# Kernel tuning notes

Measured on AMD Instinct MI355X. Metric: run time of the kernel, lower is better.

## Reference

```python
import math
import jax, jax.numpy as jnp
import numpy as np

B, N, M = 8, 2048, 1024
INPUT_SIZE = 512
HEAD_DIM = 64
NUM_HEADS = 6
ATTN_SIZE = HEAD_DIM * NUM_HEADS
MAX_CLASSES = 512


def setup_inputs() -> dict:
    key = jax.random.key(0)
    k1, k2, k3, k4, k5, k6, k7 = jax.random.split(key, 7)
    bound = 1.0 / math.sqrt(INPUT_SIZE)
    return {
        "train_embeddings": jax.random.normal(k1, (B, N, INPUT_SIZE), jnp.float32),
        "test_embeddings": jax.random.normal(k2, (B, M, INPUT_SIZE), jnp.float32),
        "targets": jax.random.randint(k3, (B, N), 0, MAX_CLASSES),
        # torch nn.Linear weights, stored as [in, out] for direct matmul
        "Wq": jax.random.uniform(k4, (INPUT_SIZE, ATTN_SIZE), jnp.float32, -bound, bound),
        "bq": jax.random.uniform(k5, (ATTN_SIZE,), jnp.float32, -bound, bound),
        "Wk": jax.random.uniform(k6, (INPUT_SIZE, ATTN_SIZE), jnp.float32, -bound, bound),
        "bk": jax.random.uniform(k7, (ATTN_SIZE,), jnp.float32, -bound, bound),
    }


def reference(train_embeddings, test_embeddings, targets, Wq, bq, Wk, bk):
    b, m, _ = test_embeddings.shape
    # projections -> [B, S, H, D]
    q_bmhd = (test_embeddings @ Wq + bq).reshape(b, m, NUM_HEADS, HEAD_DIM)
    k_bnhd = (train_embeddings @ Wk + bk).reshape(b, -1, NUM_HEADS, HEAD_DIM)
    scale = 1.0 / math.sqrt(HEAD_DIM)  # SDPA default scale
    # attention scores [B, H, M, N]
    scores = jnp.einsum("bmhd,bnhd->bhmn", q_bmhd, k_bnhd) * scale
    attn = jax.nn.softmax(scores, axis=-1)
    # one-hot train targets [B, N, C]; chunk-folding in the torch code is a
    # memory trick — mathematically it is just attn @ one_hot per head
    onehot_bnc = jax.nn.one_hot(targets, MAX_CLASSES, dtype=q_bmhd.dtype)
    out_bhmc = jnp.einsum("bhmn,bnc->bhmc", attn, onehot_bnc)
    out_bmc = out_bhmc.mean(axis=1)          # mean over heads
    out_mbc = out_bmc.transpose(1, 0, 2)      # [M, B, C]
    return jnp.log(jnp.clip(out_mbc, 1e-05) + 3e-05)
```

## Files before the change

### kernel.cpp

```cpp
#include <hip/hip_runtime.h>
#include <hip/hip_bf16.h>

#define BQ 8
#define NN 2048
#define MM 1024
#define EE 512
#define NH 6
#define AA 384
#define CC 512

#define KROW_B (AA * 2)
#define TILE_B (16 * KROW_B)
#define STILE_B (32 * KROW_B)
#define WROW_B (EE * 2)
#define WTILE_B (16 * WROW_B)

#define QSCALE 0.1803368801111204f

typedef __bf16 bf16x8 __attribute__((ext_vector_type(8)));
typedef float  f32x4  __attribute__((ext_vector_type(4)));
using bf16 = __hip_bfloat16;

static __device__ __forceinline__ f32x4 mfma16(bf16x8 a, bf16x8 b, f32x4 c) {
  return __builtin_amdgcn_mfma_f32_16x16x32_bf16(a, b, c, 0, 0, 0);
}

typedef __attribute__((address_space(1))) const void gconst_void;
typedef __attribute__((address_space(3))) void lds_void_t;
static __device__ __forceinline__ void ld_lds16(const void* g, void* l) {
  __builtin_amdgcn_global_load_lds((gconst_void*)g, (lds_void_t*)l, 16, 0, 0);
}

static __device__ __forceinline__ unsigned short f2bfu(float x) {
  union { __hip_bfloat16 h; unsigned short u; } v;
  v.h = __float2bfloat16(x);
  return v.u;
}
static __device__ __forceinline__ float bf2f(unsigned short u) {
  union { unsigned int i; float f; } x;
  x.i = ((unsigned int)u) << 16;
  return x.f;
}

__global__ __launch_bounds__(256) void transw_kernel(const float* __restrict__ W, bf16* __restrict__ WT) {
  __shared__ float t[64][65];
  int kb = (blockIdx.x / 6) * 64, nb = (blockIdx.x % 6) * 64;
  int tid = threadIdx.x;
  int lr = tid >> 4, lc = (tid & 15) * 4;
  #pragma unroll
  for (int p = 0; p < 4; p++) {
    int k = lr + p * 16;
    float4 v = *reinterpret_cast<const float4*>(W + (size_t)(kb + k) * AA + nb + lc);
    t[k][lc] = v.x; t[k][lc + 1] = v.y; t[k][lc + 2] = v.z; t[k][lc + 3] = v.w;
  }
  __syncthreads();
  #pragma unroll
  for (int p = 0; p < 4; p++) {
    int n = lr + p * 16;
    bf16* dst = WT + (size_t)(nb + n) * EE + kb + lc;
    dst[0] = __float2bfloat16(t[lc][n]);
    dst[1] = __float2bfloat16(t[lc + 1][n]);
    dst[2] = __float2bfloat16(t[lc + 2][n]);
    dst[3] = __float2bfloat16(t[lc + 3][n]);
  }
}

__global__ __launch_bounds__(512) void build_kernel(const int* __restrict__ targets,
                                                    int* __restrict__ offs, int* __restrict__ idxs) {
  __shared__ int cnt[CC], ssum[CC], pos[CC];
  int b = blockIdx.x, tid = threadIdx.x;
  cnt[tid] = 0;
  __syncthreads();
  int t[4];
  #pragma unroll
  for (int i = 0; i < 4; i++) {
    t[i] = targets[b * NN + tid * 4 + i];
    atomicAdd(&cnt[t[i]], 1);
  }
  __syncthreads();
  ssum[tid] = cnt[tid];
  __syncthreads();
  for (int d = 1; d < CC; d <<= 1) {
    int v = (tid >= d) ? ssum[tid - d] : 0;
    __syncthreads();
    ssum[tid] += v;
    __syncthreads();
  }
  int excl = ssum[tid] - cnt[tid];
  offs[b * (CC + 1) + tid] = excl;
  if (tid == CC - 1) offs[b * (CC + 1) + CC] = NN;
  pos[tid] = excl;
  __syncthreads();
  #pragma unroll
  for (int i = 0; i < 4; i++) {
    int p = atomicAdd(&pos[t[i]], 1);
    idxs[b * NN + p] = tid * 4 + i;
  }
}

__global__ __launch_bounds__(256, 3) void proj_kernel(
    const float* __restrict__ test, const float* __restrict__ train,
    const bf16* __restrict__ WqT, const bf16* __restrict__ WkT,
    const float* __restrict__ bq, const float* __restrict__ bk,
    bf16* __restrict__ Qb, bf16* __restrict__ Kb)
{
  __shared__ char wbuf[3][WTILE_B];
  int tid = threadIdx.x, wid = tid >> 6, lane = tid & 63;
  int bid = blockIdx.x;
  int sub = bid & 1, unit = bid >> 1;
  const float* A; const bf16* WT; const float* bias; bf16* C; float scale; int m0;
  if (unit < 128) { A = test;  WT = WqT; bias = bq; C = Qb; scale = QSCALE; m0 = unit * 64; }
  else            { A = train; WT = WkT; bias = bk; C = Kb; scale = 1.0f;   m0 = (unit - 128) * 64; }
  m0 += wid * 16;
  int row = lane & 15, hi = lane >> 4;

  bf16x8 af[16];
  const float* arow = A + (size_t)(m0 + row) * EE + hi * 8;
  #pragma unroll
  for (int ks = 0; ks < 16; ks++) {
    float4 u = *reinterpret_cast<const float4*>(arow + ks * 32);
    float4 v = *reinterpret_cast<const float4*>(arow + ks * 32 + 4);
    bf16x8 f;
    f[0] = (__bf16)u.x; f[1] = (__bf16)u.y; f[2] = (__bf16)u.z; f[3] = (__bf16)u.w;
    f[4] = (__bf16)v.x; f[5] = (__bf16)v.y; f[6] = (__bf16)v.z; f[7] = (__bf16)v.w;
    af[ks] = f;
  }

  int ldso[4], srco[4];
  #pragma unroll
  for (int i = 0; i < 4; i++) {
    int off = tid * 16 + i * 4096;
    int rw = off >> 10, c = off & 1023;
    ldso[i] = off;
    srco[i] = rw * WROW_B + (c ^ ((rw & 7) << 4));
  }
  const char* wgbase = (const char*)WT + (size_t)sub * 12 * WTILE_B;
  int sw = (row & 7) << 4;

  auto stage = [&](int t, int buf) {
    const char* src = wgbase + (size_t)t * WTILE_B;
    #pragma unroll
    for (int i = 0; i < 4; i++) ld_lds16(src + srco[i], wbuf[buf] + ldso[i]);
  };
  auto compute = [&](int buf, int t) {
    const char* wb = wbuf[buf] + row * WROW_B;
    f32x4 acc0 = {0.f, 0.f, 0.f, 0.f}, acc1 = {0.f, 0.f, 0.f, 0.f};
    #pragma unroll
    for (int ks = 0; ks < 16; ks += 2) {
      bf16x8 w0 = *reinterpret_cast<const bf16x8*>(wb + ((hi * 16 + ks * 64) ^ sw));
      bf16x8 w1 = *reinterpret_cast<const bf16x8*>(wb + ((hi * 16 + (ks + 1) * 64) ^ sw));
      acc0 = mfma16(af[ks], w0, acc0);
      acc1 = mfma16(af[ks + 1], w1, acc1);
    }
    f32x4 acc = acc0 + acc1;
    int ocol = (sub * 12 + t) * 16 + row;
    float bv = bias[ocol];
    #pragma unroll
    for (int j = 0; j < 4; j++)
      C[(size_t)(m0 + hi * 4 + j) * AA + ocol] = __float2bfloat16((acc[j] + bv) * scale);
  };

  stage(0, 0);
  stage(1, 1);
  asm volatile("s_waitcnt vmcnt(4)" ::: "memory");
  __builtin_amdgcn_s_barrier();
  __builtin_amdgcn_sched_barrier(0);
  stage(2, 2);
  compute(0, 0);

  int cur = 1, stg = 0;
  #pragma unroll 1
  for (int t = 1; t < 11; t++) {
    asm volatile("s_waitcnt vmcnt(8)" ::: "memory");
    __builtin_amdgcn_s_barrier();
    __builtin_amdgcn_sched_barrier(0);
    if (t < 10) stage(t + 2, stg);
    compute(cur, t);
    cur = cur + 1 < 3 ? cur + 1 : 0;
    stg = stg + 1 < 3 ? stg + 1 : 0;
  }
  asm volatile("s_waitcnt vmcnt(4)" ::: "memory");
  __builtin_amdgcn_s_barrier();
  __builtin_amdgcn_sched_barrier(0);
  compute(cur, 11);
}

__global__ __launch_bounds__(256, 3) void zpass_kernel(
    const bf16* __restrict__ Qb, const bf16* __restrict__ Kb, float* __restrict__ Zp)
{
  __shared__ char kbuf[2][STILE_B];
  int id = blockIdx.x;
  int b = id & 7, r = id >> 3, mt = r & 15, nc = r >> 4;
  int tid = threadIdx.x, wid = tid >> 6, lane = tid & 63;
  int m0 = mt * 64 + wid * 16, n0 = nc * 256;
  int row = lane & 15, hi = lane >> 4;

  bf16x8 qf[12];
  const bf16* qrow = Qb + ((size_t)(b * MM + m0 + row)) * AA + hi * 8;
  #pragma unroll
  for (int ks = 0; ks < 12; ks++) qf[ks] = *reinterpret_cast<const bf16x8*>(qrow + ks * 32);

  int ldso[6], srco[6];
  #pragma unroll
  for (int i = 0; i < 6; i++) {
    int off = tid * 16 + i * 4096;
    int rw = off / KROW_B, c = off - rw * KROW_B;
    ldso[i] = off;
    srco[i] = rw * KROW_B + (c ^ ((rw & 7) << 4));
  }
  const char* kgbase = (const char*)(Kb + ((size_t)(b * NN + n0)) * AA);

  int sw = (row & 7) << 4;
  int rbase = row * KROW_B;
  int x0 = rbase + ((hi * 16) ^ sw);
  int x1 = rbase + (((hi * 16) + 64) ^ sw);

  float zacc[NH][4];
  #pragma unroll
  for (int h = 0; h < NH; h++)
    #pragma unroll
    for (int j = 0; j < 4; j++) zacc[h][j] = 0.f;

  auto stage = [&](int t, int buf) {
    const char* src = kgbase + (size_t)t * STILE_B;
    #pragma unroll
    for (int i = 0; i < 6; i++) ld_lds16(src + srco[i], kbuf[buf] + ldso[i]);
  };
  auto compute = [&](int buf) {
    __builtin_amdgcn_s_setprio(1);
    #pragma unroll
    for (int s = 0; s < 2; s++) {
      const char* kb = kbuf[buf] + s * TILE_B;
      #pragma unroll
      for (int h = 0; h < NH; h++) {
        bf16x8 k0 = *reinterpret_cast<const bf16x8*>(kb + h * 128 + x0);
        bf16x8 k1 = *reinterpret_cast<const bf16x8*>(kb + h * 128 + x1);
        f32x4 acc = {0.f, 0.f, 0.f, 0.f};
        acc = mfma16(qf[2 * h], k0, acc);
        acc = mfma16(qf[2 * h + 1], k1, acc);
        #pragma unroll
        for (int j = 0; j < 4; j++) zacc[h][j] += __builtin_amdgcn_exp2f(acc[j]);
      }
    }
    __builtin_amdgcn_s_setprio(0);
  };

  stage(0, 0);
  asm volatile("s_waitcnt vmcnt(0)" ::: "memory");
  __builtin_amdgcn_s_barrier();
  __builtin_amdgcn_sched_barrier(0);
  stage(1, 1);
  compute(0);

  #pragma unroll 1
  for (int i = 1; i < 8; i++) {
    asm volatile("s_waitcnt vmcnt(0)" ::: "memory");
    __builtin_amdgcn_s_barrier();
    __builtin_amdgcn_sched_barrier(0);
    if (i < 7) stage(i + 1, (i + 1) & 1);
    compute(i & 1);
  }

  #pragma unroll
  for (int h = 0; h < NH; h++)
    #pragma unroll
    for (int j = 0; j < 4; j++) {
      float v = zacc[h][j];
      v += __shfl_xor(v, 1); v += __shfl_xor(v, 2);
      v += __shfl_xor(v, 4); v += __shfl_xor(v, 8);
      zacc[h][j] = v;
    }
  if (row == 0) {
    #pragma unroll
    for (int h = 0; h < NH; h++)
      #pragma unroll
      for (int j = 0; j < 4; j++)
        Zp[(((size_t)nc * 8 + b) * NH + h) * MM + m0 + hi * 4 + j] = zacc[h][j];
  }
}

__global__ __launch_bounds__(256, 3) void wpass_kernel(
    const bf16* __restrict__ Qb, const bf16* __restrict__ Kb,
    const float* __restrict__ Zp, bf16* __restrict__ W2)
{
  __shared__ char kbuf[2][STILE_B];
  int id = blockIdx.x;
  int b = id & 7, r = id >> 3, mt = r & 15, nc = r >> 4;
  int tid = threadIdx.x, wid = tid >> 6, lane = tid & 63;
  int m0 = mt * 64 + wid * 16, n0 = nc * 256;
  int row = lane & 15, hi = lane >> 4;

  bf16x8 qf[12];
  const bf16* qrow = Qb + ((size_t)(b * MM + m0 + row)) * AA + hi * 8;
  #pragma unroll
  for (int ks = 0; ks < 12; ks++) qf[ks] = *reinterpret_cast<const bf16x8*>(qrow + ks * 32);

  float rz[NH][4];
  #pragma unroll
  for (int h = 0; h < NH; h++) {
    f32x4 z = {0.f, 0.f, 0.f, 0.f};
    #pragma unroll
    for (int p = 0; p < 8; p++)
      z += *reinterpret_cast<const f32x4*>(Zp + (((size_t)p * 8 + b) * NH + h) * MM + m0 + hi * 4);
    #pragma unroll
    for (int j = 0; j < 4; j++) rz[h][j] = 1.0f / (6.0f * z[j]);
  }

  int ldso[6], srco[6];
  #pragma unroll
  for (int i = 0; i < 6; i++) {
    int off = tid * 16 + i * 4096;
    int rw = off / KROW_B, c = off - rw * KROW_B;
    ldso[i] = off;
    srco[i] = rw * KROW_B + (c ^ ((rw & 7) << 4));
  }
  const char* kgbase = (const char*)(Kb + ((size_t)(b * NN + n0)) * AA);

  int sw = (row & 7) << 4;
  int rbase = row * KROW_B;
  int x0 = rbase + ((hi * 16) ^ sw);
  int x1 = rbase + (((hi * 16) + 64) ^ sw);

  int m4 = (m0 >> 2) + hi;

  auto stage = [&](int t, int buf) {
    const char* src = kgbase + (size_t)t * STILE_B;
    #pragma unroll
    for (int i = 0; i < 6; i++) ld_lds16(src + srco[i], kbuf[buf] + ldso[i]);
  };
  auto compute = [&](int buf, int st) {
    #pragma unroll
    for (int s = 0; s < 2; s++) {
      const char* kb = kbuf[buf] + s * TILE_B;
      __builtin_amdgcn_s_setprio(1);
      float w0 = 0.f, w1 = 0.f, w2 = 0.f, w3 = 0.f;
      #pragma unroll
      for (int h = 0; h < NH; h++) {
        bf16x8 k0 = *reinterpret_cast<const bf16x8*>(kb + h * 128 + x0);
        bf16x8 k1 = *reinterpret_cast<const bf16x8*>(kb + h * 128 + x1);
        f32x4 acc = {0.f, 0.f, 0.f, 0.f};
        acc = mfma16(qf[2 * h], k0, acc);
        acc = mfma16(qf[2 * h + 1], k1, acc);
        w0 += __builtin_amdgcn_exp2f(acc[0]) * rz[h][0];
        w1 += __builtin_amdgcn_exp2f(acc[1]) * rz[h][1];
        w2 += __builtin_amdgcn_exp2f(acc[2]) * rz[h][2];
        w3 += __builtin_amdgcn_exp2f(acc[3]) * rz[h][3];
      }
      __builtin_amdgcn_s_setprio(0);
      int n = n0 + (st * 2 + s) * 16 + row;
      ushort4 q;
      q.x = f2bfu(w0); q.y = f2bfu(w1); q.z = f2bfu(w2); q.w = f2bfu(w3);
      *reinterpret_cast<ushort4*>((unsigned short*)W2 + (((size_t)(b * 256 + m4)) * NN + n) * 4) = q;
    }
  };

  stage(0, 0);
  asm volatile("s_waitcnt vmcnt(0)" ::: "memory");
  __builtin_amdgcn_s_barrier();
  __builtin_amdgcn_sched_barrier(0);
  stage(1, 1);
  compute(0, 0);

  #pragma unroll 1
  for (int i = 1; i < 8; i++) {
    asm volatile("s_waitcnt vmcnt(2)" ::: "memory");
    __builtin_amdgcn_s_barrier();
    __builtin_amdgcn_sched_barrier(0);
    if (i < 7) stage(i + 1, (i + 1) & 1);
    compute(i & 1, i);
  }
}

__global__ __launch_bounds__(512) void gather_kernel(
    const bf16* __restrict__ W2, const int* __restrict__ offs,
    const int* __restrict__ idxs, float* __restrict__ out)
{
  __shared__ char wl[2 * NN * 8];
  __shared__ int ilb[NN];
  int id = blockIdx.x;
  int b = id & 7, mt = id >> 3;
  int g0 = mt * 2;
  int tid = threadIdx.x;

  const uint4* src = (const uint4*)((const unsigned short*)W2 + ((size_t)(b * 256 + g0)) * NN * 4);
  uint4* dst = (uint4*)wl;
  #pragma unroll
  for (int i = tid; i < 2 * NN * 8 / 16; i += 512) dst[i] = src[i];
  const int* il = idxs + b * NN;
  #pragma unroll
  for (int i = tid; i < NN; i += 512) ilb[i] = il[i];
  __syncthreads();

  int c = tid;
  int o0 = offs[b * (CC + 1) + c], o1 = offs[b * (CC + 1) + c + 1];
  #pragma unroll 1
  for (int g = 0; g < 2; g++) {
    float s0 = 0.f, s1 = 0.f, s2 = 0.f, s3 = 0.f;
    for (int i = o0; i < o1; i++) {
      int idx = ilb[i];
      ushort4 v = *reinterpret_cast<const ushort4*>(wl + g * (NN * 8) + idx * 8);
      s0 += bf2f(v.x); s1 += bf2f(v.y); s2 += bf2f(v.z); s3 += bf2f(v.w);
    }
    int m = mt * 8 + g * 4;
    out[((size_t)(m + 0) * BQ + b) * CC + c] = __logf(fmaxf(s0, 1e-5f) + 3e-5f);
    out[((size_t)(m + 1) * BQ + b) * CC + c] = __logf(fmaxf(s1, 1e-5f) + 3e-5f);
    out[((size_t)(m + 2) * BQ + b) * CC + c] = __logf(fmaxf(s2, 1e-5f) + 3e-5f);
    out[((size_t)(m + 3) * BQ + b) * CC + c] = __logf(fmaxf(s3, 1e-5f) + 3e-5f);
  }
}

extern "C" void kernel_launch(void* const* d_in, const int* in_sizes, int n_in,
                              void* d_out, int out_size, void* d_ws, size_t ws_size,
                              hipStream_t stream) {
  const float* train = (const float*)d_in[0];
  const float* test  = (const float*)d_in[1];
  const int*   tgt   = (const int*)d_in[2];
  const float* Wq    = (const float*)d_in[3];
  const float* bq    = (const float*)d_in[4];
  const float* Wk    = (const float*)d_in[5];
  const float* bk    = (const float*)d_in[6];
  float* out = (float*)d_out;

  char* ws = (char*)d_ws;
  bf16*  WqT  = (bf16*)(ws);
  bf16*  WkT  = (bf16*)(ws + 393216);
  bf16*  Qb   = (bf16*)(ws + 786432);
  bf16*  Kb   = (bf16*)(ws + 7077888);
  float* Zp   = (float*)(ws + 19660800);
  bf16*  Wbuf = (bf16*)(ws + 21233664);
  int*   offs = (int*)(ws + 54788096);
  int*   idxs = (int*)(ws + 54804512);

  transw_kernel<<<48, 256, 0, stream>>>(Wq, WqT);
  transw_kernel<<<48, 256, 0, stream>>>(Wk, WkT);
  build_kernel<<<BQ, 512, 0, stream>>>(tgt, offs, idxs);
  proj_kernel<<<768, 256, 0, stream>>>(test, train, WqT, WkT, bq, bk, Qb, Kb);
  zpass_kernel<<<1024, 256, 0, stream>>>(Qb, Kb, Zp);
  wpass_kernel<<<1024, 256, 0, stream>>>(Qb, Kb, Zp, Wbuf);
  gather_kernel<<<1024, 512, 0, stream>>>(Wbuf, offs, idxs, out);
}
```

Measured before the change: 112.3 us.

## Double per-wave M rows in zpass/wpass to reuse K tiles; merge transpose launches

Each wave in zpass and wpass now covers 32 query rows instead of 16. It holds two sets of Q fragments and reuses every K fragment read from LDS for two MFMAs, so the grid halves and LDS and global K traffic per output falls. The two weight-transpose launches are merged into a single 96-block launch to save one launch. In exchange, register pressure rises (launch bounds drop to 2 blocks per CU), there are fewer blocks to fill the GPU, and the wpass wait count is relaxed to match the extra stores.

```diff
diff --git a/kernel.cpp b/kernel.cpp
--- a/kernel.cpp
+++ b/kernel.cpp
@@ -42,9 +42,15 @@
   return x.f;
 }
 
-__global__ __launch_bounds__(256) void transw_kernel(const float* __restrict__ W, bf16* __restrict__ WT) {
+__global__ __launch_bounds__(256) void transw_kernel(
+    const float* __restrict__ Wq, const float* __restrict__ Wk,
+    bf16* __restrict__ WqT, bf16* __restrict__ WkT) {
   __shared__ float t[64][65];
-  int kb = (blockIdx.x / 6) * 64, nb = (blockIdx.x % 6) * 64;
+  int id = blockIdx.x;
+  const float* W = (id < 48) ? Wq : Wk;
+  bf16* WT = (id < 48) ? WqT : WkT;
+  if (id >= 48) id -= 48;
+  int kb = (id / 6) * 64, nb = (id % 6) * 64;
   int tid = threadIdx.x;
   int lr = tid >> 4, lc = (tid & 15) * 4;
   #pragma unroll
@@ -185,20 +191,23 @@
   compute(cur, 11);
 }
 
-__global__ __launch_bounds__(256, 3) void zpass_kernel(
+__global__ __launch_bounds__(256, 2) void zpass_kernel(
     const bf16* __restrict__ Qb, const bf16* __restrict__ Kb, float* __restrict__ Zp)
 {
   __shared__ char kbuf[2][STILE_B];
   int id = blockIdx.x;
-  int b = id & 7, r = id >> 3, mt = r & 15, nc = r >> 4;
+  int b = id & 7, r = id >> 3, mt = r & 7, nc = r >> 3;
   int tid = threadIdx.x, wid = tid >> 6, lane = tid & 63;
-  int m0 = mt * 64 + wid * 16, n0 = nc * 256;
+  int m0 = mt * 128 + wid * 32, n0 = nc * 256;
   int row = lane & 15, hi = lane >> 4;
 
-  bf16x8 qf[12];
-  const bf16* qrow = Qb + ((size_t)(b * MM + m0 + row)) * AA + hi * 8;
-  #pragma unroll
-  for (int ks = 0; ks < 12; ks++) qf[ks] = *reinterpret_cast<const bf16x8*>(qrow + ks * 32);
+  bf16x8 qf[2][12];
+  #pragma unroll
+  for (int s = 0; s < 2; s++) {
+    const bf16* qrow = Qb + ((size_t)(b * MM + m0 + s * 16 + row)) * AA + hi * 8;
+    #pragma unroll
+    for (int ks = 0; ks < 12; ks++) qf[s][ks] = *reinterpret_cast<const bf16x8*>(qrow + ks * 32);
+  }
 
   int ldso[6], srco[6];
   #pragma unroll
@@ -215,11 +224,13 @@
   int x0 = rbase + ((hi * 16) ^ sw);
   int x1 = rbase + (((hi * 16) + 64) ^ sw);
 
-  float zacc[NH][4];
-  #pragma unroll
-  for (int h = 0; h < NH; h++)
-    #pragma unroll
-    for (int j = 0; j < 4; j++) zacc[h][j] = 0.f;
+  float zacc[2][NH][4];
+  #pragma unroll
+  for (int s = 0; s < 2; s++)
+    #pragma unroll
+    for (int h = 0; h < NH; h++)
+      #pragma unroll
+      for (int j = 0; j < 4; j++) zacc[s][h][j] = 0.f;
 
   auto stage = [&](int t, int buf) {
     const char* src = kgbase + (size_t)t * STILE_B;
@@ -229,17 +240,22 @@
   auto compute = [&](int buf) {
     __builtin_amdgcn_s_setprio(1);
     #pragma unroll
-    for (int s = 0; s < 2; s++) {
-      const char* kb = kbuf[buf] + s * TILE_B;
+    for (int sub = 0; sub < 2; sub++) {
+      const char* kb = kbuf[buf] + sub * TILE_B;
       #pragma unroll
       for (int h = 0; h < NH; h++) {
         bf16x8 k0 = *reinterpret_cast<const bf16x8*>(kb + h * 128 + x0);
         bf16x8 k1 = *reinterpret_cast<const bf16x8*>(kb + h * 128 + x1);
-        f32x4 acc = {0.f, 0.f, 0.f, 0.f};
-        acc = mfma16(qf[2 * h], k0, acc);
-        acc = mfma16(qf[2 * h + 1], k1, acc);
+        f32x4 a0 = {0.f, 0.f, 0.f, 0.f}, a1 = {0.f, 0.f, 0.f, 0.f};
+        a0 = mfma16(qf[0][2 * h], k0, a0);
+        a1 = mfma16(qf[1][2 * h], k0, a1);
+        a0 = mfma16(qf[0][2 * h + 1], k1, a0);
+        a1 = mfma16(qf[1][2 * h + 1], k1, a1);
         #pragma unroll
-        for (int j = 0; j < 4; j++) zacc[h][j] += __builtin_amdgcn_exp2f(acc[j]);
+        for (int j = 0; j < 4; j++) {
+          zacc[0][h][j] += __builtin_amdgcn_exp2f(a0[j]);
+          zacc[1][h][j] += __builtin_amdgcn_exp2f(a1[j]);
+        }
       }
     }
     __builtin_amdgcn_s_setprio(0);
@@ -262,49 +278,58 @@
   }
 
   #pragma unroll
-  for (int h = 0; h < NH; h++)
-    #pragma unroll
-    for (int j = 0; j < 4; j++) {
-      float v = zacc[h][j];
-      v += __shfl_xor(v, 1); v += __shfl_xor(v, 2);
-      v += __shfl_xor(v, 4); v += __shfl_xor(v, 8);
-      zacc[h][j] = v;
-    }
+  for (int s = 0; s < 2; s++)
+    #pragma unroll
+    for (int h = 0; h < NH; h++)
+      #pragma unroll
+      for (int j = 0; j < 4; j++) {
+        float v = zacc[s][h][j];
+        v += __shfl_xor(v, 1); v += __shfl_xor(v, 2);
+        v += __shfl_xor(v, 4); v += __shfl_xor(v, 8);
+        zacc[s][h][j] = v;
+      }
   if (row == 0) {
     #pragma unroll
-    for (int h = 0; h < NH; h++)
-      #pragma unroll
-      for (int j = 0; j < 4; j++)
-        Zp[(((size_t)nc * 8 + b) * NH + h) * MM + m0 + hi * 4 + j] = zacc[h][j];
-  }
-}
-
-__global__ __launch_bounds__(256, 3) void wpass_kernel(
+    for (int s = 0; s < 2; s++)
+      #pragma unroll
+      for (int h = 0; h < NH; h++)
+        #pragma unroll
+        for (int j = 0; j < 4; j++)
+          Zp[(((size_t)nc * 8 + b) * NH + h) * MM + m0 + s * 16 + hi * 4 + j] = zacc[s][h][j];
+  }
+}
+
+__global__ __launch_bounds__(256, 2) void wpass_kernel(
     const bf16* __restrict__ Qb, const bf16* __restrict__ Kb,
     const float* __restrict__ Zp, bf16* __restrict__ W2)
 {
   __shared__ char kbuf[2][STILE_B];
   int id = blockIdx.x;
-  int b = id & 7, r = id >> 3, mt = r & 15, nc = r >> 4;
+  int b = id & 7, r = id >> 3, mt = r & 7, nc = r >> 3;
   int tid = threadIdx.x, wid = tid >> 6, lane = tid & 63;
-  int m0 = mt * 64 + wid * 16, n0 = nc * 256;
+  int m0 = mt * 128 + wid * 32, n0 = nc * 256;
   int row = lane & 15, hi = lane >> 4;
 
-  bf16x8 qf[12];
-  const bf16* qrow = Qb + ((size_t)(b * MM + m0 + row)) * AA + hi * 8;
-  #pragma unroll
-  for (int ks = 0; ks < 12; ks++) qf[ks] = *reinterpret_cast<const bf16x8*>(qrow + ks * 32);
-
-  float rz[NH][4];
-  #pragma unroll
-  for (int h = 0; h < NH; h++) {
-    f32x4 z = {0.f, 0.f, 0.f, 0.f};
-    #pragma unroll
-    for (int p = 0; p < 8; p++)
-      z += *reinterpret_cast<const f32x4*>(Zp + (((size_t)p * 8 + b) * NH + h) * MM + m0 + hi * 4);
-    #pragma unroll
-    for (int j = 0; j < 4; j++) rz[h][j] = 1.0f / (6.0f * z[j]);
-  }
+  bf16x8 qf[2][12];
+  #pragma unroll
+  for (int s = 0; s < 2; s++) {
+    const bf16* qrow = Qb + ((size_t)(b * MM + m0 + s * 16 + row)) * AA + hi * 8;
+    #pragma unroll
+    for (int ks = 0; ks < 12; ks++) qf[s][ks] = *reinterpret_cast<const bf16x8*>(qrow + ks * 32);
+  }
+
+  float rz[2][NH][4];
+  #pragma unroll
+  for (int s = 0; s < 2; s++)
+    #pragma unroll
+    for (int h = 0; h < NH; h++) {
+      f32x4 z = {0.f, 0.f, 0.f, 0.f};
+      #pragma unroll
+      for (int p = 0; p < 8; p++)
+        z += *reinterpret_cast<const f32x4*>(Zp + (((size_t)p * 8 + b) * NH + h) * MM + m0 + s * 16 + hi * 4);
+      #pragma unroll
+      for (int j = 0; j < 4; j++) rz[s][h][j] = 1.0f / (6.0f * z[j]);
+    }
 
   int ldso[6], srco[6];
   #pragma unroll
@@ -321,7 +346,8 @@
   int x0 = rbase + ((hi * 16) ^ sw);
   int x1 = rbase + (((hi * 16) + 64) ^ sw);
 
-  int m4 = (m0 >> 2) + hi;
+  int m4a = (m0 >> 2) + hi;
+  int m4b = ((m0 + 16) >> 2) + hi;
 
   auto stage = [&](int t, int buf) {
     const char* src = kgbase + (size_t)t * STILE_B;
@@ -330,27 +356,36 @@
   };
   auto compute = [&](int buf, int st) {
     #pragma unroll
-    for (int s = 0; s < 2; s++) {
-      const char* kb = kbuf[buf] + s * TILE_B;
+    for (int sub = 0; sub < 2; sub++) {
+      const char* kb = kbuf[buf] + sub * TILE_B;
       __builtin_amdgcn_s_setprio(1);
-      float w0 = 0.f, w1 = 0.f, w2 = 0.f, w3 = 0.f;
+      float w0a = 0.f, w1a = 0.f, w2a = 0.f, w3a = 0.f;
+      float w0b = 0.f, w1b = 0.f, w2b = 0.f, w3b = 0.f;
       #pragma unroll
       for (int h = 0; h < NH; h++) {
         bf16x8 k0 = *reinterpret_cast<const bf16x8*>(kb + h * 128 + x0);
         bf16x8 k1 = *reinterpret_cast<const bf16x8*>(kb + h * 128 + x1);
-        f32x4 acc = {0.f, 0.f, 0.f, 0.f};
-        acc = mfma16(qf[2 * h], k0, acc);
-        acc = mfma16(qf[2 * h + 1], k1, acc);
-        w0 += __builtin_amdgcn_exp2f(acc[0]) * rz[h][0];
-        w1 += __builtin_amdgcn_exp2f(acc[1]) * rz[h][1];
-        w2 += __builtin_amdgcn_exp2f(acc[2]) * rz[h][2];
-        w3 += __builtin_amdgcn_exp2f(acc[3]) * rz[h][3];
+        f32x4 a0 = {0.f, 0.f, 0.f, 0.f}, a1 = {0.f, 0.f, 0.f, 0.f};
+        a0 = mfma16(qf[0][2 * h], k0, a0);
+        a1 = mfma16(qf[1][2 * h], k0, a1);
+        a0 = mfma16(qf[0][2 * h + 1], k1, a0);
+        a1 = mfma16(qf[1][2 * h + 1], k1, a1);
+        w0a += __builtin_amdgcn_exp2f(a0[0]) * rz[0][h][0];
+        w1a += __builtin_amdgcn_exp2f(a0[1]) * rz[0][h][1];
+        w2a += __builtin_amdgcn_exp2f(a0[2]) * rz[0][h][2];
+        w3a += __builtin_amdgcn_exp2f(a0[3]) * rz[0][h][3];
+        w0b += __builtin_amdgcn_exp2f(a1[0]) * rz[1][h][0];
+        w1b += __builtin_amdgcn_exp2f(a1[1]) * rz[1][h][1];
+        w2b += __builtin_amdgcn_exp2f(a1[2]) * rz[1][h][2];
+        w3b += __builtin_amdgcn_exp2f(a1[3]) * rz[1][h][3];
       }
       __builtin_amdgcn_s_setprio(0);
-      int n = n0 + (st * 2 + s) * 16 + row;
-      ushort4 q;
-      q.x = f2bfu(w0); q.y = f2bfu(w1); q.z = f2bfu(w2); q.w = f2bfu(w3);
-      *reinterpret_cast<ushort4*>((unsigned short*)W2 + (((size_t)(b * 256 + m4)) * NN + n) * 4) = q;
+      int n = n0 + (st * 2 + sub) * 16 + row;
+      ushort4 qa, qb2;
+      qa.x = f2bfu(w0a); qa.y = f2bfu(w1a); qa.z = f2bfu(w2a); qa.w = f2bfu(w3a);
+      qb2.x = f2bfu(w0b); qb2.y = f2bfu(w1b); qb2.z = f2bfu(w2b); qb2.w = f2bfu(w3b);
+      *reinterpret_cast<ushort4*>((unsigned short*)W2 + (((size_t)(b * 256 + m4a)) * NN + n) * 4) = qa;
+      *reinterpret_cast<ushort4*>((unsigned short*)W2 + (((size_t)(b * 256 + m4b)) * NN + n) * 4) = qb2;
     }
   };
 
@@ -363,7 +398,7 @@
 
   #pragma unroll 1
   for (int i = 1; i < 8; i++) {
-    asm volatile("s_waitcnt vmcnt(2)" ::: "memory");
+    asm volatile("s_waitcnt vmcnt(4)" ::: "memory");
     __builtin_amdgcn_s_barrier();
     __builtin_amdgcn_sched_barrier(0);
     if (i < 7) stage(i + 1, (i + 1) & 1);
@@ -431,11 +466,10 @@
   int*   offs = (int*)(ws + 54788096);
   int*   idxs = (int*)(ws + 54804512);
 
-  transw_kernel<<<48, 256, 0, stream>>>(Wq, WqT);
-  transw_kernel<<<48, 256, 0, stream>>>(Wk, WkT);
+  transw_kernel<<<96, 256, 0, stream>>>(Wq, Wk, WqT, WkT);
   build_kernel<<<BQ, 512, 0, stream>>>(tgt, offs, idxs);
   proj_kernel<<<768, 256, 0, stream>>>(test, train, WqT, WkT, bq, bk, Qb, Kb);
-  zpass_kernel<<<1024, 256, 0, stream>>>(Qb, Kb, Zp);
-  wpass_kernel<<<1024, 256, 0, stream>>>(Qb, Kb, Zp, Wbuf);
+  zpass_kernel<<<512, 256, 0, stream>>>(Qb, Kb, Zp);
+  wpass_kernel<<<512, 256, 0, stream>>>(Qb, Kb, Zp, Wbuf);
   gather_kernel<<<1024, 512, 0, stream>>>(Wbuf, offs, idxs, out);
 }
```

Result: faster. 108.4 us (-3.4%).
